# Kernel tuning notes

Measured on AMD Instinct MI355X. Metric: run time of the kernel, lower is better.

Reference implementation:

```python
import jax, jax.numpy as jnp
import numpy as np

B, S_ENC, S_DEC, D_IN, UNITS = 8, 2048, 1024, 512, 512

def setup_inputs() -> dict:
    key = jax.random.key(0)
    k1, k2, k3, k4, k5 = jax.random.split(key, 5)
    scale = 1.0 / np.sqrt(D_IN)
    return {
        "encoding": jax.random.normal(k1, (B, S_ENC, D_IN), dtype=jnp.float32),
        "decoding": jax.random.normal(k2, (B, S_DEC, D_IN), dtype=jnp.float32),
        "Wq": jax.random.normal(k3, (D_IN, UNITS), dtype=jnp.float32) * scale,
        "Wk": jax.random.normal(k4, (D_IN, UNITS), dtype=jnp.float32) * scale,
        "Wv": jax.random.normal(k5, (D_IN, UNITS), dtype=jnp.float32) * scale,
    }

def reference(encoding, decoding, Wq, Wk, Wv):
    # bias-free projections
    q = jnp.einsum('bsd,du->bsu', decoding, Wq)   # [B, S_dec, U]
    k = jnp.einsum('bsd,du->bsu', encoding, Wk)   # [B, S_enc, U]
    v = jnp.einsum('bsd,du->bsu', encoding, Wv)   # [B, S_enc, U]
    # NOTE: original applies no 1/sqrt(d) scaling
    score = jnp.einsum('bqu,bku->bqk', q, k)      # [B, S_dec, S_enc]
    score = jax.nn.softmax(score, axis=2)
    return jnp.einsum('bqk,bku->bqu', score, v)   # [B, S_dec, U]
```

## Files before the change

### kernel.cpp

```cpp
#include <hip/hip_runtime.h>
#include <hip/hip_bf16.h>


typedef __attribute__((ext_vector_type(8))) _Float16 f16x8;
typedef __attribute__((ext_vector_type(4))) _Float16 f16x4;
typedef __attribute__((ext_vector_type(4))) float f32x4;

#define MFMA16(a, b, c) __builtin_amdgcn_mfma_f32_16x16x32_f16(a, b, c, 0, 0, 0)

__device__ __forceinline__ void glds16(const void* g, void* l) {
    __builtin_amdgcn_global_load_lds(
        (const __attribute__((address_space(1))) void*)g,
        (__attribute__((address_space(3))) void*)l, 16, 0, 0);
}

__global__ __launch_bounds__(256) void convert_f16(const float* __restrict__ x,
                                                   _Float16* __restrict__ o) {
    size_t i = ((size_t)blockIdx.x * 256 + threadIdx.x) * 8;
    float4 a0 = *(const float4*)(x + i);
    float4 a1 = *(const float4*)(x + i + 4);
    float v[8] = {a0.x, a0.y, a0.z, a0.w, a1.x, a1.y, a1.z, a1.w};
    f16x8 h;
#pragma unroll
    for (int j = 0; j < 8; ++j) h[j] = (_Float16)v[j];
    *(f16x8*)(o + i) = h;
}

__global__ __launch_bounds__(256) void wtrans_kernel(const float* __restrict__ Wq,
                                                     const float* __restrict__ Wk,
                                                     const float* __restrict__ Wv,
                                                     _Float16* __restrict__ planes) {
    const float* W = blockIdx.z == 0 ? Wq : (blockIdx.z == 1 ? Wk : Wv);
    _Float16* ot = planes + (size_t)blockIdx.z * 262144;
    __shared__ float T[64][65];
    const int d0 = blockIdx.y * 64, u0 = blockIdx.x * 64;
    const int tr = threadIdx.x >> 4, tc = (threadIdx.x & 15) * 4;
#pragma unroll
    for (int j = 0; j < 4; ++j) {
        float4 vv = *(const float4*)(W + (size_t)(d0 + tr + j * 16) * 512 + u0 + tc);
        T[tr + j * 16][tc + 0] = vv.x;
        T[tr + j * 16][tc + 1] = vv.y;
        T[tr + j * 16][tc + 2] = vv.z;
        T[tr + j * 16][tc + 3] = vv.w;
    }
    __syncthreads();
#pragma unroll
    for (int j = 0; j < 4; ++j) {
        int ul = tr + j * 16;
        f16x4 h;
#pragma unroll
        for (int i = 0; i < 4; ++i) h[i] = (_Float16)T[tc + i][ul];
        *(f16x4*)(ot + (size_t)(u0 + ul) * 512 + d0 + tc) = h;
    }
}

template <int BM, int BN, int OUT>
__global__ __launch_bounds__(256) void gemm_kernel(
    const _Float16* __restrict__ A, const _Float16* __restrict__ B,
    void* __restrict__ O1,
    int lda, int ldb, int K, int a_row_batch, long b_batch, int ldo) {
    constexpr int ASZ = BM * 64, BSZ = BN * 64;
    constexpr int BUFSZ = ASZ + BSZ;
    constexpr int MT = BM / 32, NT = BN / 32;
    constexpr int JA = BM / 64, JB = BN / 64;
    __shared__ __align__(16) char smem[2 * BUFSZ];

    const int tid = threadIdx.x;
    const int wave = tid >> 6, lane = tid & 63;
    const int quad = lane >> 4, m16 = lane & 15;
    const int wr = wave >> 1, wc = wave & 1;
    const int z = blockIdx.z;
    const int row0 = z * a_row_batch + blockIdx.y * BM;
    const int col0 = blockIdx.x * BN;

    const int srowA = wave * (16 * JA) + (lane >> 2);
    const int srowB = wave * (16 * JB) + (lane >> 2);
    const int scol = (lane & 3) * 8;
    const _Float16* agp = A + (size_t)(row0 + srowA) * lda + scol;
    const _Float16* bgp = B + (size_t)z * b_batch + (size_t)(col0 + srowB) * ldb + scol;
    const int ldsAoff = wave * (1024 * JA);
    const int ldsBoff = ASZ + wave * (1024 * JB);

    f32x4 acc[MT][NT];
#pragma unroll
    for (int mt = 0; mt < MT; ++mt)
#pragma unroll
        for (int nt = 0; nt < NT; ++nt) acc[mt][nt] = (f32x4){0.f, 0.f, 0.f, 0.f};

    const int nIter = K / 32;
    auto stage = [&](int i, int buf) {
        char* base = smem + buf * BUFSZ;
        const int k0 = i * 32;
#pragma unroll
        for (int j = 0; j < JA; ++j)
            glds16(agp + k0 + j * 16 * lda, base + ldsAoff + j * 1024);
#pragma unroll
        for (int j = 0; j < JB; ++j)
            glds16(bgp + k0 + j * 16 * ldb, base + ldsBoff + j * 1024);
    };

    stage(0, 0);
    for (int i = 0; i < nIter; ++i) {
        __syncthreads();
        if (i + 1 < nIter) stage(i + 1, (i + 1) & 1);
        const char* bb = smem + (i & 1) * BUFSZ;
        const char* pa = bb + (wr * (BM / 2) + m16) * 64 + quad * 16;
        const char* pb = bb + ASZ + (wc * (BN / 2) + m16) * 64 + quad * 16;
        f16x8 af[MT];
#pragma unroll
        for (int mt = 0; mt < MT; ++mt) af[mt] = *(const f16x8*)(pa + mt * 1024);
#pragma unroll
        for (int nt = 0; nt < NT; ++nt) {
            f16x8 bf = *(const f16x8*)(pb + nt * 1024);
#pragma unroll
            for (int mt = 0; mt < MT; ++mt) acc[mt][nt] = MFMA16(af[mt], bf, acc[mt][nt]);
        }
    }

    if (OUT == 0) {
        _Float16* o = (_Float16*)O1;
#pragma unroll
        for (int mt = 0; mt < MT; ++mt)
#pragma unroll
            for (int nt = 0; nt < NT; ++nt)
#pragma unroll
                for (int rr = 0; rr < 4; ++rr) {
                    int row = row0 + wr * (BM / 2) + mt * 16 + quad * 4 + rr;
                    int col = col0 + wc * (BN / 2) + nt * 16 + m16;
                    o[(size_t)row * ldo + col] = (_Float16)acc[mt][nt][rr];
                }
    } else if (OUT == 2) {
        float* o = (float*)O1;
#pragma unroll
        for (int mt = 0; mt < MT; ++mt)
#pragma unroll
            for (int nt = 0; nt < NT; ++nt)
#pragma unroll
                for (int rr = 0; rr < 4; ++rr) {
                    int row = row0 + wr * (BM / 2) + mt * 16 + quad * 4 + rr;
                    int col = col0 + wc * (BN / 2) + nt * 16 + m16;
                    o[(size_t)row * ldo + col] = acc[mt][nt][rr];
                }
    } else {
        _Float16* vtp = (_Float16*)O1;
        const int row0g = blockIdx.y * 128;
        const int b = row0g >> 11;
        const int s_base = (row0g & 2047) + wr * 64;
        char* reg = smem + wave * 4096;
#pragma unroll
        for (int p = 0; p < 2; ++p) {
            __syncthreads();
#pragma unroll
            for (int nt2 = 0; nt2 < 2; ++nt2) {
                int nt = p * 2 + nt2;
#pragma unroll
                for (int mt = 0; mt < 4; ++mt) {
                    f16x4 pk;
#pragma unroll
                    for (int rr = 0; rr < 4; ++rr) pk[rr] = (_Float16)acc[mt][nt][rr];
                    *(f16x4*)(reg + (nt2 * 16 + m16) * 128 + (mt * 16 + quad * 4) * 2) = pk;
                }
            }
            __syncthreads();
            const int u_base = col0 + wc * 64 + p * 32;
#pragma unroll
            for (int j = 0; j < 4; ++j) {
                int n = j * 8 + (lane >> 3);
                int mo = (lane & 7) * 8;
                f16x8 val = *(const f16x8*)(reg + n * 128 + mo * 2);
                *(f16x8*)(vtp + (size_t)(b * 512 + u_base + n) * 2048 + s_base + mo) = val;
            }
        }
    }
}

__global__ __launch_bounds__(256) void softmax_kernel(const float* __restrict__ S,
                                                      _Float16* __restrict__ P) {
    const int row = blockIdx.x;
    const int tid = threadIdx.x;
    const int wave = tid >> 6, lane = tid & 63;
    __shared__ float red[8];

    const float* sp = S + (size_t)row * 2048 + tid * 8;
    float4 x0 = *(const float4*)sp;
    float4 x1 = *(const float4*)(sp + 4);
    float v[8] = {x0.x, x0.y, x0.z, x0.w, x1.x, x1.y, x1.z, x1.w};

    float mx = v[0];
#pragma unroll
    for (int i = 1; i < 8; ++i) mx = fmaxf(mx, v[i]);
#pragma unroll
    for (int off = 32; off > 0; off >>= 1) mx = fmaxf(mx, __shfl_down(mx, off));
    if (lane == 0) red[wave] = mx;
    __syncthreads();
    if (tid == 0) red[4] = fmaxf(fmaxf(red[0], red[1]), fmaxf(red[2], red[3]));
    __syncthreads();
    mx = red[4];

    float e[8];
    float sum = 0.f;
#pragma unroll
    for (int i = 0; i < 8; ++i) {
        e[i] = exp2f((v[i] - mx) * 1.44269504088896f);
        sum += e[i];
    }
#pragma unroll
    for (int off = 32; off > 0; off >>= 1) sum += __shfl_down(sum, off);
    if (lane == 0) red[wave] = sum;
    __syncthreads();
    if (tid == 0) red[5] = red[0] + red[1] + red[2] + red[3];
    __syncthreads();
    float inv = 1.0f / red[5];

    f16x8 ov;
#pragma unroll
    for (int i = 0; i < 8; ++i) ov[i] = (_Float16)(e[i] * inv);
    *(f16x8*)(P + (size_t)row * 2048 + tid * 8) = ov;
}

extern "C" void kernel_launch(void* const* d_in, const int* in_sizes, int n_in,
                              void* d_out, int out_size, void* d_ws, size_t ws_size,
                              hipStream_t stream) {
    const float* enc = (const float*)d_in[0];
    const float* dec = (const float*)d_in[1];
    const float* Wq = (const float*)d_in[2];
    const float* Wk = (const float*)d_in[3];
    const float* Wv = (const float*)d_in[4];
    float* out = (float*)d_out;

    char* ws = (char*)d_ws;
    _Float16* qh = (_Float16*)(ws);
    _Float16* kh = (_Float16*)(ws + ((size_t)8 << 20));
    _Float16* P = (_Float16*)(ws);
    _Float16* vt = (_Float16*)(ws + ((size_t)32 << 20));
    float* S = (float*)(ws + ((size_t)48 << 20));
    _Float16* dech = (_Float16*)(ws + ((size_t)48 << 20));
    _Float16* wts = (_Float16*)(ws + ((size_t)56 << 20));
    _Float16* ench = (_Float16*)(ws + ((size_t)112 << 20));

    dim3 blk(256);
    convert_f16<<<4096, blk, 0, stream>>>(enc, ench);
    convert_f16<<<2048, blk, 0, stream>>>(dec, dech);
    wtrans_kernel<<<dim3(8, 8, 3), blk, 0, stream>>>(Wq, Wk, Wv, wts);
    gemm_kernel<64, 128, 0><<<dim3(4, 128, 1), blk, 0, stream>>>(
        dech, wts, qh, 512, 512, 512, 0, 0, 512);
    gemm_kernel<64, 128, 0><<<dim3(4, 256, 1), blk, 0, stream>>>(
        ench, wts + 262144, kh, 512, 512, 512, 0, 0, 512);
    gemm_kernel<128, 128, 1><<<dim3(4, 128, 1), blk, 0, stream>>>(
        ench, wts + 524288, vt, 512, 512, 512, 0, 0, 0);
    gemm_kernel<128, 128, 2><<<dim3(16, 8, 8), blk, 0, stream>>>(
        qh, kh, S, 512, 512, 512, 1024, (long)2048 * 512, 2048);
    softmax_kernel<<<8192, blk, 0, stream>>>(S, P);
    gemm_kernel<64, 64, 2><<<dim3(8, 16, 8), blk, 0, stream>>>(
        P, vt, out, 2048, 2048, 2048, 1024, (long)512 * 2048, 512);
}
```

Before: 246.4 us.

## Fuse softmax exponentiation into PV matmul using precomputed row stats

Replaces the softmax kernel that wrote a normalized fp16 P matrix with a stats kernel that only stores each row's max and inverse sum. A new PV kernel then reads the fp32 scores directly, exponentiates them in registers, multiplies them by V with MFMA, and scales the result by the inverse sum. It also merges the two input conversion kernels into a single launch. This removes the P write and read round trip, but the PV kernel loads fp32 S straight from global memory with no LDS tiling, repeats the exp for every one of the 8 column tiles, and runs only 512 blocks, so it may become memory or compute bound.

```diff
diff --git a/kernel.cpp b/kernel.cpp
--- a/kernel.cpp
+++ b/kernel.cpp
@@ -7,6 +7,7 @@
 typedef __attribute__((ext_vector_type(4))) float f32x4;
 
 #define MFMA16(a, b, c) __builtin_amdgcn_mfma_f32_16x16x32_f16(a, b, c, 0, 0, 0)
+#define L2E 1.44269504088896f
 
 __device__ __forceinline__ void glds16(const void* g, void* l) {
     __builtin_amdgcn_global_load_lds(
@@ -14,9 +15,16 @@
         (__attribute__((address_space(3))) void*)l, 16, 0, 0);
 }
 
-__global__ __launch_bounds__(256) void convert_f16(const float* __restrict__ x,
-                                                   _Float16* __restrict__ o) {
-    size_t i = ((size_t)blockIdx.x * 256 + threadIdx.x) * 8;
+__global__ __launch_bounds__(256) void convert_all(const float* __restrict__ enc,
+                                                   const float* __restrict__ dec,
+                                                   _Float16* __restrict__ oenc,
+                                                   _Float16* __restrict__ odec) {
+    const int b = blockIdx.x;
+    const float* x;
+    _Float16* o;
+    size_t i;
+    if (b < 4096) { x = enc; o = oenc; i = ((size_t)b * 256 + threadIdx.x) * 8; }
+    else          { x = dec; o = odec; i = ((size_t)(b - 4096) * 256 + threadIdx.x) * 8; }
     float4 a0 = *(const float4*)(x + i);
     float4 a1 = *(const float4*)(x + i + 4);
     float v[8] = {a0.x, a0.y, a0.z, a0.w, a1.x, a1.y, a1.z, a1.w};
@@ -174,8 +182,9 @@
     }
 }
 
-__global__ __launch_bounds__(256) void softmax_kernel(const float* __restrict__ S,
-                                                      _Float16* __restrict__ P) {
+__global__ __launch_bounds__(256) void stats_kernel(const float* __restrict__ S,
+                                                    float* __restrict__ m_,
+                                                    float* __restrict__ linv_) {
     const int row = blockIdx.x;
     const int tid = threadIdx.x;
     const int wave = tid >> 6, lane = tid & 63;
@@ -197,25 +206,99 @@
     __syncthreads();
     mx = red[4];
 
-    float e[8];
     float sum = 0.f;
 #pragma unroll
-    for (int i = 0; i < 8; ++i) {
-        e[i] = exp2f((v[i] - mx) * 1.44269504088896f);
-        sum += e[i];
-    }
+    for (int i = 0; i < 8; ++i) sum += exp2f((v[i] - mx) * L2E);
 #pragma unroll
     for (int off = 32; off > 0; off >>= 1) sum += __shfl_down(sum, off);
     if (lane == 0) red[wave] = sum;
     __syncthreads();
-    if (tid == 0) red[5] = red[0] + red[1] + red[2] + red[3];
-    __syncthreads();
-    float inv = 1.0f / red[5];
-
-    f16x8 ov;
-#pragma unroll
-    for (int i = 0; i < 8; ++i) ov[i] = (_Float16)(e[i] * inv);
-    *(f16x8*)(P + (size_t)row * 2048 + tid * 8) = ov;
+    if (tid == 0) {
+        m_[row] = mx;
+        linv_[row] = 1.0f / (red[0] + red[1] + red[2] + red[3]);
+    }
+}
+
+__global__ __launch_bounds__(256) void pv_kernel(
+    const float* __restrict__ S, const _Float16* __restrict__ vt,
+    const float* __restrict__ m_, const float* __restrict__ linv_,
+    float* __restrict__ out) {
+    const int wid = blockIdx.x * 4 + (threadIdx.x >> 6);
+    const int lane = threadIdx.x & 63;
+    const int quad = lane >> 4, m16 = lane & 15;
+    const int ntile = wid & 7;
+    const int mtile = wid >> 3;
+    const int row0 = mtile * 32;
+    const int z = row0 >> 10;
+    const int u0 = ntile * 64;
+
+    const float* srow[2];
+    float mrow[2];
+#pragma unroll
+    for (int mf = 0; mf < 2; ++mf) {
+        srow[mf] = S + (size_t)(row0 + mf * 16 + m16) * 2048 + quad * 8;
+        mrow[mf] = m_[row0 + mf * 16 + m16];
+    }
+    const _Float16* vrow[4];
+#pragma unroll
+    for (int nf = 0; nf < 4; ++nf)
+        vrow[nf] = vt + (size_t)(z * 512 + u0 + nf * 16 + m16) * 2048 + quad * 8;
+
+    f32x4 acc[2][4];
+#pragma unroll
+    for (int mf = 0; mf < 2; ++mf)
+#pragma unroll
+        for (int nf = 0; nf < 4; ++nf) acc[mf][nf] = (f32x4){0.f, 0.f, 0.f, 0.f};
+
+    float4 Ab[2][2][2];
+    f16x8 Bb[2][4];
+#pragma unroll
+    for (int mf = 0; mf < 2; ++mf) {
+        Ab[0][mf][0] = *(const float4*)(srow[mf]);
+        Ab[0][mf][1] = *(const float4*)(srow[mf] + 4);
+    }
+#pragma unroll
+    for (int nf = 0; nf < 4; ++nf) Bb[0][nf] = *(const f16x8*)(vrow[nf]);
+
+#pragma unroll 2
+    for (int i = 0; i < 64; ++i) {
+        const int cur = i & 1, nxt = cur ^ 1;
+        if (i + 1 < 64) {
+            const int k = (i + 1) * 32;
+#pragma unroll
+            for (int mf = 0; mf < 2; ++mf) {
+                Ab[nxt][mf][0] = *(const float4*)(srow[mf] + k);
+                Ab[nxt][mf][1] = *(const float4*)(srow[mf] + k + 4);
+            }
+#pragma unroll
+            for (int nf = 0; nf < 4; ++nf) Bb[nxt][nf] = *(const f16x8*)(vrow[nf] + k);
+        }
+        f16x8 a16[2];
+#pragma unroll
+        for (int mf = 0; mf < 2; ++mf) {
+#pragma unroll
+            for (int j = 0; j < 4; ++j) {
+                a16[mf][j] = (_Float16)exp2f((Ab[cur][mf][0][j] - mrow[mf]) * L2E);
+                a16[mf][j + 4] = (_Float16)exp2f((Ab[cur][mf][1][j] - mrow[mf]) * L2E);
+            }
+        }
+#pragma unroll
+        for (int nf = 0; nf < 4; ++nf)
+#pragma unroll
+            for (int mf = 0; mf < 2; ++mf)
+                acc[mf][nf] = MFMA16(a16[mf], Bb[cur][nf], acc[mf][nf]);
+    }
+
+#pragma unroll
+    for (int mf = 0; mf < 2; ++mf)
+#pragma unroll
+        for (int rr = 0; rr < 4; ++rr) {
+            const int grow = row0 + mf * 16 + quad * 4 + rr;
+            const float li = linv_[grow];
+#pragma unroll
+            for (int nf = 0; nf < 4; ++nf)
+                out[(size_t)grow * 512 + u0 + nf * 16 + m16] = acc[mf][nf][rr] * li;
+        }
 }
 
 extern "C" void kernel_launch(void* const* d_in, const int* in_sizes, int n_in,
@@ -231,16 +314,16 @@
     char* ws = (char*)d_ws;
     _Float16* qh = (_Float16*)(ws);
     _Float16* kh = (_Float16*)(ws + ((size_t)8 << 20));
-    _Float16* P = (_Float16*)(ws);
     _Float16* vt = (_Float16*)(ws + ((size_t)32 << 20));
     float* S = (float*)(ws + ((size_t)48 << 20));
     _Float16* dech = (_Float16*)(ws + ((size_t)48 << 20));
     _Float16* wts = (_Float16*)(ws + ((size_t)56 << 20));
     _Float16* ench = (_Float16*)(ws + ((size_t)112 << 20));
+    float* m_ = (float*)(ws + ((size_t)112 << 20));
+    float* linv_ = (float*)(ws + ((size_t)112 << 20) + 32768);
 
     dim3 blk(256);
-    convert_f16<<<4096, blk, 0, stream>>>(enc, ench);
-    convert_f16<<<2048, blk, 0, stream>>>(dec, dech);
+    convert_all<<<6144, blk, 0, stream>>>(enc, dec, ench, dech);
     wtrans_kernel<<<dim3(8, 8, 3), blk, 0, stream>>>(Wq, Wk, Wv, wts);
     gemm_kernel<64, 128, 0><<<dim3(4, 128, 1), blk, 0, stream>>>(
         dech, wts, qh, 512, 512, 512, 0, 0, 512);
@@ -250,7 +333,6 @@
         ench, wts + 524288, vt, 512, 512, 512, 0, 0, 0);
     gemm_kernel<128, 128, 2><<<dim3(16, 8, 8), blk, 0, stream>>>(
         qh, kh, S, 512, 512, 512, 1024, (long)2048 * 512, 2048);
-    softmax_kernel<<<8192, blk, 0, stream>>>(S, P);
-    gemm_kernel<64, 64, 2><<<dim3(8, 16, 8), blk, 0, stream>>>(
-        P, vt, out, 2048, 2048, 2048, 1024, (long)512 * 2048, 512);
-}
+    stats_kernel<<<8192, blk, 0, stream>>>(S, m_, linv_);
+    pv_kernel<<<512, blk, 0, stream>>>(S, vt, m_, linv_, out);
+}
```

After: 307.9 us. 25.0% more time.
